# Kernel optimization log

Hardware: AMD Instinct MI355X
Metric: run time of the kernel (lower is better)

The kernel has to match this reference:

```python
import jax, jax.numpy as jnp
import numpy as np

B, T = 2, 2048
TOK, POS = 512, 512          # d_model = TOK + POS = 1024
H, D, KVH = 16, 64, 4        # inner_dim = 1024, kv_inner = 256, kv_repeat = 4


def setup_inputs() -> dict:
    key = jax.random.key(0)
    ks = jax.random.split(key, 7)
    def w(k, shape, fan_in):
        return jax.random.normal(k, shape, jnp.float32) / np.float32(np.sqrt(fan_in))
    x = jax.random.normal(ks[0], (B, T, TOK + POS), jnp.float32)
    Wq = w(ks[1], (POS, H * D), POS)          # q_proj (qk_source='pos')
    Wk = w(ks[2], (POS, KVH * D), POS)        # k_proj (GQA)
    Wv = w(ks[3], (TOK, KVH * D), TOK)        # v_proj from token subspace
    Wo = w(ks[4], (H * D, TOK + POS), H * D)  # out_proj -> d_model
    q_phase_angle = 0.1 * jax.random.normal(ks[5], (H,), jnp.float32)
    alibi_log_slopes = jnp.full((H,), np.float32(np.log(np.log(10.0))))
    return dict(x=x, Wq=Wq, Wk=Wk, Wv=Wv, Wo=Wo,
                q_phase_angle=q_phase_angle, alibi_log_slopes=alibi_log_slopes)


def reference(x, Wq, Wk, Wv, Wo, q_phase_angle, alibi_log_slopes):
    b, t, _ = x.shape
    x_tok = x[:, :, :TOK]
    x_pos = x[:, :, TOK:]
    # Q/K from positional subspace, V from token subspace
    q = (x_pos @ Wq).reshape(b, t, H, D).transpose(0, 2, 1, 3)      # (B,H,T,D)
    k = (x_pos @ Wk).reshape(b, t, KVH, D).transpose(0, 2, 1, 3)    # (B,KVH,T,D)
    v = (x_tok @ Wv).reshape(b, t, KVH, D).transpose(0, 2, 1, 3)
    # per-head 2D q-phase rotation over consecutive dim pairs
    c = jnp.cos(q_phase_angle)[None, :, None, None]
    s = jnp.sin(q_phase_angle)[None, :, None, None]
    q2 = q.reshape(b, H, t, D // 2, 2)
    q0, q1 = q2[..., 0], q2[..., 1]
    q = jnp.stack([q0 * c - q1 * s, q0 * s + q1 * c], axis=-1).reshape(b, H, t, D)
    # GQA: repeat each kv head kv_repeat times (consecutively, matching torch expand+reshape)
    rep = H // KVH
    k = jnp.repeat(k, rep, axis=1)
    v = jnp.repeat(v, rep, axis=1)
    att = jnp.einsum('bhqd,bhkd->bhqk', q, k) / np.float32(np.sqrt(D))
    # ALiBi: rel_pos[i,j] = i - j, slope = exp(log_slope)
    pos = jnp.arange(t)
    rel = (pos[:, None] - pos[None, :]).astype(jnp.float32)
    att = att + jnp.exp(alibi_log_slopes)[None, :, None, None] * rel[None, None]
    # causal mask
    mask = pos[:, None] >= pos[None, :]
    att = jnp.where(mask[None, None], att, -jnp.inf)
    # softmax1: exp(att - max) / (1 + sum exp(att - max))  (exactly as the torch code)
    m = jnp.max(att, axis=-1, keepdims=True)
    e = jnp.exp(att - m)
    att = e / (1.0 + jnp.sum(e, axis=-1, keepdims=True))
    out = jnp.einsum('bhqk,bhkd->bhqd', att, v)
    out = out.transpose(0, 2, 1, 3).reshape(b, t, H * D)
    return out @ Wo
```

## Files before the change

### kernel.cpp

```cpp
#include <hip/hip_runtime.h>
#include <hip/hip_bf16.h>
#include <math.h>

#define B_   2
#define T_   2048
#define TOK_ 512
#define POS_ 512
#define H_   16
#define D_   64
#define KVH_ 4

typedef float f32x4 __attribute__((ext_vector_type(4)));
typedef short bf16x8 __attribute__((ext_vector_type(8)));
typedef unsigned short u16;
typedef u16 u16x4 __attribute__((ext_vector_type(4)));
typedef u16 u16x8 __attribute__((ext_vector_type(8)));

__device__ inline u16 f2bf(float f) {
    union { float f; unsigned u; } v; v.f = f;
    unsigned r = v.u + 0x7FFFu + ((v.u >> 16) & 1u);
    return (u16)(r >> 16);
}

__global__ void cvt_x(const float* __restrict__ X, u16* __restrict__ Xb) {
    int i = (blockIdx.x * 256 + threadIdx.x) * 4;
    f32x4 v = *reinterpret_cast<const f32x4*>(X + i);
    u16x4 o;
    #pragma unroll
    for (int u = 0; u < 4; ++u) o[u] = f2bf(v[u]);
    *reinterpret_cast<u16x4*>(Xb + i) = o;
}

__global__ void transp_k(const float* __restrict__ W, u16* __restrict__ WT,
                         int K, int N) {
    __shared__ float t[32][33];
    const int tid = threadIdx.x;
    const int k0 = blockIdx.y * 32, n0 = blockIdx.x * 32;
    const int r = tid >> 3, c4 = (tid & 7) * 4;
    f32x4 v = *reinterpret_cast<const f32x4*>(W + (size_t)(k0 + r) * N + n0 + c4);
    #pragma unroll
    for (int u = 0; u < 4; ++u) t[r][c4 + u] = v[u];
    __syncthreads();
    u16x4 o;
    #pragma unroll
    for (int u = 0; u < 4; ++u) o[u] = f2bf(t[c4 + u][r]);
    *reinterpret_cast<u16x4*>(WT + (size_t)(n0 + r) * K + k0 + c4) = o;
}

template<int MODE>
__global__ __launch_bounds__(256, 2)
void mfma_gemm(const u16* __restrict__ A, int lda, int aoff,
               const u16* __restrict__ Bt, int Ktot,
               void* __restrict__ Cout, const float* __restrict__ angles)
{
    __shared__ __align__(16) unsigned char lds[20480];
    unsigned char* As = lds;
    unsigned char* Bs = lds + 10240;

    const int tid  = threadIdx.x;
    const int lane = tid & 63;
    const int w    = tid >> 6;
    const int wm   = w >> 1, wn = w & 1;
    const int lr   = lane & 15, lg = lane >> 4;
    const int m0   = blockIdx.y * 128;
    const int n0   = blockIdx.x * 128;

    f32x4 acc[4][4] = {};

    for (int k0 = 0; k0 < Ktot; k0 += 32) {
        __syncthreads();
        #pragma unroll
        for (int p = 0; p < 2; ++p) {
            int lin = tid + p * 256;
            int row = lin >> 2;
            int kc  = (lin & 3) * 8;
            u16x8 av = *reinterpret_cast<const u16x8*>(
                A + (size_t)(m0 + row) * lda + aoff + k0 + kc);
            *reinterpret_cast<u16x8*>(As + row * 80 + kc * 2) = av;
            u16x8 bv = *reinterpret_cast<const u16x8*>(
                Bt + (size_t)(n0 + row) * Ktot + k0 + kc);
            *reinterpret_cast<u16x8*>(Bs + row * 80 + kc * 2) = bv;
        }
        __syncthreads();

        bf16x8 af[4], bfr[4];
        #pragma unroll
        for (int mt = 0; mt < 4; ++mt)
            af[mt] = *reinterpret_cast<bf16x8*>(
                As + (wm * 64 + mt * 16 + lr) * 80 + lg * 16);
        #pragma unroll
        for (int nt = 0; nt < 4; ++nt)
            bfr[nt] = *reinterpret_cast<bf16x8*>(
                Bs + (wn * 64 + nt * 16 + lr) * 80 + lg * 16);
        #pragma unroll
        for (int mt = 0; mt < 4; ++mt)
            #pragma unroll
            for (int nt = 0; nt < 4; ++nt)
                acc[mt][nt] = __builtin_amdgcn_mfma_f32_16x16x32_bf16(
                    af[mt], bfr[nt], acc[mt][nt], 0, 0, 0);
    }

    #pragma unroll
    for (int nt = 0; nt < 4; ++nt) {
        const int nbase = n0 + wn * 64 + nt * 16;
        float ca = 0.f, sa = 0.f;
        if (MODE == 1) {
            const int h = nbase >> 6;
            ca = cosf(angles[h]);
            sa = sinf(angles[h]);
        }
        #pragma unroll
        for (int mt = 0; mt < 4; ++mt) {
            #pragma unroll
            for (int j = 0; j < 4; ++j) {
                const int m = m0 + wm * 64 + mt * 16 + lg * 4 + j;
                const int n = nbase + lr;
                const float v = acc[mt][nt][j];
                if (MODE == 0) {
                    ((float*)Cout)[(size_t)m * (TOK_ + POS_) + n] = v;
                } else if (MODE == 1) {
                    const float p = __shfl_xor(v, 1);
                    const float o = (lr & 1) ? (p * sa + v * ca)
                                             : (v * ca - p * sa);
                    const int b = m >> 11, t = m & (T_ - 1);
                    const int h = n >> 6, d = n & 63;
                    ((u16*)Cout)[(((size_t)(b * H_ + h)) * T_ + t) * D_ + d] = f2bf(o);
                } else {
                    const int b = m >> 11, t = m & (T_ - 1);
                    const int h = n >> 6, d = n & 63;
                    ((u16*)Cout)[(((size_t)(b * KVH_ + h)) * T_ + t) * D_ + d] = f2bf(v);
                }
            }
        }
    }
}

__global__ __launch_bounds__(256, 3)
void flash_mfma(const u16* __restrict__ Q, const u16* __restrict__ K,
                const u16* __restrict__ V, const float* __restrict__ slopes,
                u16* __restrict__ O)
{
    __shared__ __align__(16) unsigned char lds[24576];
    unsigned char* Ks = lds;
    unsigned char* Vt = lds + 8192;
    unsigned char* Ps = lds + 16384;

    const int tid  = threadIdx.x;
    const int lane = tid & 63;
    const int w    = tid >> 6;
    const int lr   = lane & 15;
    const int lg   = lane >> 4;

    const int bh  = blockIdx.y;
    const int b   = bh >> 4;
    const int h   = bh & 15;
    const int kvh = h >> 2;

    const float slope = expf(slopes[h]);

    const u16* Kp = K + ((size_t)(b * KVH_ + kvh)) * T_ * D_;
    const u16* Vp = V + ((size_t)(b * KVH_ + kvh)) * T_ * D_;

    unsigned char* Pw = Ps + w * 2048;

    #pragma unroll 1
    for (int pass = 0; pass < 2; ++pass) {
        const int qt = pass ? (T_ / 64 - 1 - blockIdx.x) : blockIdx.x;
        const int q0 = qt * 64;

        const u16* Qp = Q + (((size_t)(b * H_ + h)) * T_ + q0 + w * 16) * D_;
        const bf16x8 qa0 = *reinterpret_cast<const bf16x8*>(Qp + lr * D_ + lg * 8);
        const bf16x8 qa1 = *reinterpret_cast<const bf16x8*>(Qp + lr * D_ + 32 + lg * 8);

        f32x4 acc[4] = {};
        float mrow[4], lrow[4];
        #pragma unroll
        for (int j = 0; j < 4; ++j) { mrow[j] = -INFINITY; lrow[j] = 0.f; }

        for (int jt = 0; jt <= qt; ++jt) {
            const int kv0 = jt * 64;
            __syncthreads();
            #pragma unroll
            for (int it = 0; it < 2; ++it) {
                int lin = tid + it * 256;
                int row = lin >> 3;
                int c16 = (lin & 7) * 16;
                u16x8 kv = *reinterpret_cast<const u16x8*>(
                    Kp + (size_t)(kv0 + row) * D_ + (lin & 7) * 8);
                *reinterpret_cast<u16x8*>(Ks + ((row * 128 + c16) ^ ((row & 7) << 4))) = kv;
                int key = lin & 63;
                int d8  = (lin >> 6) * 8;
                u16x8 vv = *reinterpret_cast<const u16x8*>(
                    Vp + (size_t)(kv0 + key) * D_ + d8);
                #pragma unroll
                for (int e = 0; e < 8; ++e) {
                    int d = d8 + e;
                    *reinterpret_cast<u16*>(
                        Vt + ((d * 128 + key * 2) ^ ((d & 7) << 4))) = (u16)vv[e];
                }
            }
            __syncthreads();

            f32x4 s[4];
            #pragma unroll
            for (int n = 0; n < 4; ++n) {
                int krow = n * 16 + lr;
                int swz  = (krow & 7) << 4;
                bf16x8 kb0 = *reinterpret_cast<bf16x8*>(Ks + ((krow * 128 + lg * 16) ^ swz));
                bf16x8 kb1 = *reinterpret_cast<bf16x8*>(Ks + ((krow * 128 + 64 + lg * 16) ^ swz));
                f32x4 z = {};
                z    = __builtin_amdgcn_mfma_f32_16x16x32_bf16(qa0, kb0, z, 0, 0, 0);
                s[n] = __builtin_amdgcn_mfma_f32_16x16x32_bf16(qa1, kb1, z, 0, 0, 0);
            }

            const int qbase = q0 + w * 16 + lg * 4;
            #pragma unroll
            for (int j = 0; j < 4; ++j) {
                const int qr = qbase + j;
                float a[4];
                float tmax = -INFINITY;
                #pragma unroll
                for (int n = 0; n < 4; ++n) {
                    int kg = kv0 + n * 16 + lr;
                    float vsc = s[n][j] * 0.125f + slope * (float)(qr - kg);
                    vsc = (kg <= qr) ? vsc : -INFINITY;
                    a[n] = vsc;
                    tmax = fmaxf(tmax, vsc);
                }
                #pragma unroll
                for (int off = 1; off < 16; off <<= 1)
                    tmax = fmaxf(tmax, __shfl_xor(tmax, off));
                const float mnew = fmaxf(mrow[j], tmax);
                const float sc   = __expf(mrow[j] - mnew);
                float rsum = 0.f;
                u16 pb[4];
                #pragma unroll
                for (int n = 0; n < 4; ++n) {
                    float p = __expf(a[n] - mnew);
                    rsum += p;
                    pb[n] = f2bf(p);
                }
                #pragma unroll
                for (int off = 1; off < 16; off <<= 1)
                    rsum += __shfl_xor(rsum, off);
                lrow[j] = lrow[j] * sc + rsum;
                mrow[j] = mnew;
                #pragma unroll
                for (int dt = 0; dt < 4; ++dt) acc[dt][j] *= sc;
                const int prow = lg * 4 + j;
                #pragma unroll
                for (int n = 0; n < 4; ++n)
                    *reinterpret_cast<u16*>(
                        Pw + ((prow * 128 + (n * 16 + lr) * 2) ^ ((prow & 7) << 4))) = pb[n];
            }

            #pragma unroll
            for (int kh = 0; kh < 2; ++kh) {
                bf16x8 pa = *reinterpret_cast<bf16x8*>(
                    Pw + ((lr * 128 + kh * 64 + lg * 16) ^ ((lr & 7) << 4)));
                #pragma unroll
                for (int dt = 0; dt < 4; ++dt) {
                    int drow = dt * 16 + lr;
                    bf16x8 vb = *reinterpret_cast<bf16x8*>(
                        Vt + ((drow * 128 + kh * 64 + lg * 16) ^ ((drow & 7) << 4)));
                    acc[dt] = __builtin_amdgcn_mfma_f32_16x16x32_bf16(pa, vb, acc[dt], 0, 0, 0);
                }
            }
        }

        u16* Op = O + ((size_t)b * T_ + q0 + w * 16) * (H_ * D_) + h * 64;
        #pragma unroll
        for (int j = 0; j < 4; ++j) {
            const float inv = 1.0f / (1.0f + lrow[j]);
            const int r = lg * 4 + j;
            #pragma unroll
            for (int dt = 0; dt < 4; ++dt)
                Op[(size_t)r * (H_ * D_) + dt * 16 + lr] = f2bf(acc[dt][j] * inv);
        }
    }
}

extern "C" void kernel_launch(void* const* d_in, const int* in_sizes, int n_in,
                              void* d_out, int out_size, void* d_ws, size_t ws_size,
                              hipStream_t stream)
{
    const float* x      = (const float*)d_in[0];
    const float* Wq     = (const float*)d_in[1];
    const float* Wk     = (const float*)d_in[2];
    const float* Wv     = (const float*)d_in[3];
    const float* Wo     = (const float*)d_in[4];
    const float* ang    = (const float*)d_in[5];
    const float* slopes = (const float*)d_in[6];
    float* out = (float*)d_out;

    u16* xb   = (u16*)d_ws;
    u16* Qb   = xb   + (size_t)4096 * 1024;
    u16* Kb   = Qb   + (size_t)B_ * H_ * T_ * D_;
    u16* Vb   = Kb   + (size_t)B_ * KVH_ * T_ * D_;
    u16* AttO = Vb   + (size_t)B_ * KVH_ * T_ * D_;
    u16* WqT  = AttO + (size_t)4096 * 1024;
    u16* WkT  = WqT  + (size_t)1024 * 512;
    u16* WvT  = WkT  + (size_t)256 * 512;
    u16* WoT  = WvT  + (size_t)256 * 512;

    cvt_x<<<4096, 256, 0, stream>>>(x, xb);
    transp_k<<<dim3(1024 / 32, 512 / 32), 256, 0, stream>>>(Wq, WqT, 512, 1024);
    transp_k<<<dim3(256 / 32, 512 / 32), 256, 0, stream>>>(Wk, WkT, 512, 256);
    transp_k<<<dim3(256 / 32, 512 / 32), 256, 0, stream>>>(Wv, WvT, 512, 256);
    transp_k<<<dim3(1024 / 32, 1024 / 32), 256, 0, stream>>>(Wo, WoT, 1024, 1024);

    mfma_gemm<1><<<dim3(8, 32), 256, 0, stream>>>(xb, 1024, 512, WqT, 512, Qb, ang);
    mfma_gemm<2><<<dim3(2, 32), 256, 0, stream>>>(xb, 1024, 512, WkT, 512, Kb, nullptr);
    mfma_gemm<2><<<dim3(2, 32), 256, 0, stream>>>(xb, 1024, 0,   WvT, 512, Vb, nullptr);

    flash_mfma<<<dim3(T_ / 128, B_ * H_), 256, 0, stream>>>(Qb, Kb, Vb, slopes, AttO);

    mfma_gemm<0><<<dim3(8, 32), 256, 0, stream>>>(AttO, 1024, 0, WoT, 1024, out, nullptr);
}
```

Before: 239.6 us.

## Double-buffer K/V tiles in LDS with register prefetch in flash attention

Adds a second LDS buffer for K and transposed V. The next tile's global loads are issued into registers at the top of each iteration and written to the alternate buffer after the MFMA work, so each iteration needs one barrier instead of two. The aim is to hide global-load latency behind the QK and PV compute. In exchange, LDS use grows from 24 KB to 40 KB, launch bounds drop from 3 to 2 blocks per CU, and register pressure rises from the prefetch registers.

```diff
diff --git a/kernel.cpp b/kernel.cpp
--- a/kernel.cpp
+++ b/kernel.cpp
@@ -135,15 +135,52 @@
     }
 }
 
-__global__ __launch_bounds__(256, 3)
+__device__ inline void stage_load(const u16* __restrict__ Kp,
+                                  const u16* __restrict__ Vp,
+                                  int kv0, int tid,
+                                  u16x8* kreg, u16x8* vreg)
+{
+    #pragma unroll
+    for (int it = 0; it < 2; ++it) {
+        int lin = tid + it * 256;
+        int row = lin >> 3;
+        kreg[it] = *reinterpret_cast<const u16x8*>(
+            Kp + (size_t)(kv0 + row) * D_ + (lin & 7) * 8);
+        int key = lin & 63;
+        int d8  = (lin >> 6) * 8;
+        vreg[it] = *reinterpret_cast<const u16x8*>(
+            Vp + (size_t)(kv0 + key) * D_ + d8);
+    }
+}
+
+__device__ inline void stage_write(unsigned char* __restrict__ Ksb,
+                                   unsigned char* __restrict__ Vtb,
+                                   int tid, const u16x8* kreg, const u16x8* vreg)
+{
+    #pragma unroll
+    for (int it = 0; it < 2; ++it) {
+        int lin = tid + it * 256;
+        int row = lin >> 3;
+        int c16 = (lin & 7) * 16;
+        *reinterpret_cast<u16x8*>(Ksb + ((row * 128 + c16) ^ ((row & 7) << 4))) = kreg[it];
+        int key = lin & 63;
+        int d8  = (lin >> 6) * 8;
+        #pragma unroll
+        for (int e = 0; e < 8; ++e) {
+            int d = d8 + e;
+            *reinterpret_cast<u16*>(
+                Vtb + ((d * 128 + key * 2) ^ ((d & 7) << 4))) = (u16)vreg[it][e];
+        }
+    }
+}
+
+__global__ __launch_bounds__(256, 2)
 void flash_mfma(const u16* __restrict__ Q, const u16* __restrict__ K,
                 const u16* __restrict__ V, const float* __restrict__ slopes,
                 u16* __restrict__ O)
 {
-    __shared__ __align__(16) unsigned char lds[24576];
-    unsigned char* Ks = lds;
-    unsigned char* Vt = lds + 8192;
-    unsigned char* Ps = lds + 16384;
+    __shared__ __align__(16) unsigned char lds[40960];
+    unsigned char* Ps = lds + 32768;
 
     const int tid  = threadIdx.x;
     const int lane = tid & 63;
@@ -163,6 +200,9 @@
 
     unsigned char* Pw = Ps + w * 2048;
 
+    u16x8 kreg[2], vreg[2];
+    int cur = 0;
+
     #pragma unroll 1
     for (int pass = 0; pass < 2; ++pass) {
         const int qt = pass ? (T_ / 64 - 1 - blockIdx.x) : blockIdx.x;
@@ -177,29 +217,18 @@
         #pragma unroll
         for (int j = 0; j < 4; ++j) { mrow[j] = -INFINITY; lrow[j] = 0.f; }
 
+        stage_load(Kp, Vp, 0, tid, kreg, vreg);
+        __syncthreads();
+        stage_write(lds + cur * 8192, lds + 16384 + cur * 8192, tid, kreg, vreg);
+
         for (int jt = 0; jt <= qt; ++jt) {
+            __syncthreads();
+            if (jt < qt)
+                stage_load(Kp, Vp, (jt + 1) * 64, tid, kreg, vreg);
+
+            unsigned char* Ks = lds + cur * 8192;
+            unsigned char* Vt = lds + 16384 + cur * 8192;
             const int kv0 = jt * 64;
-            __syncthreads();
-            #pragma unroll
-            for (int it = 0; it < 2; ++it) {
-                int lin = tid + it * 256;
-                int row = lin >> 3;
-                int c16 = (lin & 7) * 16;
-                u16x8 kv = *reinterpret_cast<const u16x8*>(
-                    Kp + (size_t)(kv0 + row) * D_ + (lin & 7) * 8);
-                *reinterpret_cast<u16x8*>(Ks + ((row * 128 + c16) ^ ((row & 7) << 4))) = kv;
-                int key = lin & 63;
-                int d8  = (lin >> 6) * 8;
-                u16x8 vv = *reinterpret_cast<const u16x8*>(
-                    Vp + (size_t)(kv0 + key) * D_ + d8);
-                #pragma unroll
-                for (int e = 0; e < 8; ++e) {
-                    int d = d8 + e;
-                    *reinterpret_cast<u16*>(
-                        Vt + ((d * 128 + key * 2) ^ ((d & 7) << 4))) = (u16)vv[e];
-                }
-            }
-            __syncthreads();
 
             f32x4 s[4];
             #pragma unroll
@@ -265,6 +294,12 @@
                         Vt + ((drow * 128 + kh * 64 + lg * 16) ^ ((drow & 7) << 4)));
                     acc[dt] = __builtin_amdgcn_mfma_f32_16x16x32_bf16(pa, vb, acc[dt], 0, 0, 0);
                 }
+            }
+
+            if (jt < qt) {
+                stage_write(lds + (cur ^ 1) * 8192, lds + 16384 + (cur ^ 1) * 8192,
+                            tid, kreg, vreg);
+                cur ^= 1;
             }
         }
 
```

After: 236.1 us. No clear change (-1.5%).
